# Kernel tuning notes

Measured on AMD Instinct MI355X. Metric: run time of the kernel, lower is better.

## Reference

```python
import jax, jax.numpy as jnp
import numpy as np
from functools import partial

BIG = 1e9  # placeholder squared distance for 'no surface voxel here'


def _surface(fg):
    """Boundary voxels: foreground with at least one 4-neighbor background (image border counts as background)."""
    p = jnp.pad(fg, 1)  # pads with False
    interior = p[:-2, 1:-1] & p[2:, 1:-1] & p[1:-1, :-2] & p[1:-1, 2:]
    return fg & ~interior


def _edt(mask):
    """Exact Euclidean distance transform (unit spacing, matching spacing_mm=(1,1,1)).
    Separable two-pass: 1D squared distance along rows, then combine along columns.
    mask: [H, W] bool -> dist: [H, W] float32 distance to nearest True voxel."""
    H, W = mask.shape
    i = jnp.arange(H, dtype=jnp.float32)
    j = jnp.arange(W, dtype=jnp.float32)
    d1 = (i[:, None] - i[None, :]) ** 2                      # [H, H]
    pen = jnp.where(mask, 0.0, BIG).astype(jnp.float32)      # [H, W]
    g = jnp.min(d1[:, :, None] + pen[None, :, :], axis=1)    # [H, W] (min over source row i')
    d2 = (j[:, None] - j[None, :]) ** 2                      # [W, W]
    f = jnp.min(g[:, None, :] + d2[None, :, :], axis=2)      # [H, W] (min over source col j')
    return jnp.sqrt(f)


def _percentile(d, mask, pct):
    """pct-percentile of d over voxels where mask is True (inf if mask empty)."""
    vals = jnp.sort(jnp.where(mask, d, jnp.inf).ravel())
    n = jnp.sum(mask)
    idx = jnp.clip(jnp.ceil(pct / 100.0 * n.astype(jnp.float32)).astype(jnp.int32) - 1,
                   0, vals.size - 1)
    return jnp.where(n > 0, vals[idx], jnp.inf)


def _pair_hd(pred_m, gt_m):
    """Robust Hausdorff (100th and 95th percentile) between surfaces of two binary masks."""
    sp = _surface(pred_m)
    sg = _surface(gt_m)
    dt_to_pred = _edt(sp)  # distance of every voxel to pred surface
    dt_to_gt = _edt(sg)    # distance of every voxel to gt surface

    def robust(p):
        return jnp.maximum(_percentile(dt_to_pred, sg, p),   # gt -> pred
                           _percentile(dt_to_gt, sp, p))     # pred -> gt

    return jnp.stack([robust(100.0), robust(95.0)])  # [2]


def _forward(logits, target):
    num_classes = logits.shape[1]
    probs = jax.nn.softmax(logits, axis=1)
    pred = jnp.argmax(probs, axis=1)  # [B, H, W]
    classes = jnp.arange(1, num_classes)  # include_background=False -> drop class 0
    pred_oh = pred[:, None, :, :] == classes[None, :, None, None]    # [B, Cfg, H, W] bool
    tgt_oh = target[:, None, :, :] == classes[None, :, None, None]   # [B, Cfg, H, W] bool

    def per_image(args):
        pm, tm = args  # each [Cfg, H, W]
        return jax.vmap(_pair_hd)(pm, tm)  # [Cfg, 2]

    res = jax.lax.map(per_image, (pred_oh, tgt_oh))  # [B, Cfg, 2]
    # average='micro': mean over all (batch, class) pairs
    return jnp.mean(res, axis=(0, 1))  # [2] = (hd100, hd95)


def setup_inputs() -> dict:
    key = jax.random.key(0)
    k1, k2 = jax.random.split(key)
    B, C, H, W = 8, 4, 192, 192
    logits = jax.random.normal(k1, (B, C, H, W), dtype=jnp.float32)
    target = jax.random.randint(k2, (B, H, W), 0, C, dtype=jnp.int64)
    return {"logits": logits, "target": target}


def reference(logits, target):
    return _forward(logits, target)
```

## Files before the change

### kernel.cpp

```cpp
#include <hip/hip_runtime.h>
#include <hip/hip_bf16.h>
#include <math.h>
#include <stdint.h>
#include <limits.h>

#define BB 8
#define NC 4
#define HH 192
#define WW 192
#define HWP (HH * WW)
#define NPAIR 24
#define NPD 48
#define NWRD 576
#define NCHUNK 16
#define WPC (NWRD / NCHUNK)
#define NBIN 4096
#define BIGI 1000000000

typedef unsigned long long u64;

__global__ void k_prep(const float* __restrict__ logits, const int* __restrict__ target,
                       u64* __restrict__ fgbits, unsigned* __restrict__ ghist,
                       int* __restrict__ ovfcnt, int* __restrict__ ovfmax) {
    int idx = blockIdx.x * 256 + threadIdx.x;
    if (idx < NPD * NBIN) ghist[idx] = 0;
    if (blockIdx.x == 1151) {
        if (threadIdx.x < NPD) ovfcnt[threadIdx.x] = 0;
        else if (threadIdx.x >= 64 && threadIdx.x < 64 + NPD) ovfmax[threadIdx.x - 64] = 0;
    }
    int b = idx / HWP;
    int p = idx - b * HWP;
    const float* base = logits + (size_t)b * NC * HWP + p;
    float l0 = base[0], l1 = base[HWP], l2 = base[2 * HWP], l3 = base[3 * HWP];
    int pred = 0; float best = l0;
    if (l1 > best) { best = l1; pred = 1; }
    if (l2 > best) { best = l2; pred = 2; }
    if (l3 > best) { best = l3; pred = 3; }
    int t = target[(size_t)b * HWP + p];
    int lane = threadIdx.x & 63;
    int g = p >> 6;
#pragma unroll
    for (int cls = 1; cls <= 3; ++cls) {
        u64 mp = __ballot(pred == cls);
        u64 mt = __ballot(t == cls);
        if (lane == 0) {
            int pair = b * 3 + (cls - 1);
            fgbits[(size_t)(pair * 2 + 0) * NWRD + g] = mp;
            fgbits[(size_t)(pair * 2 + 1) * NWRD + g] = mt;
        }
    }
}

__device__ __forceinline__ u64 surf_word(const u64* F, int i, int k) {
    u64 r0 = F[i * 3], r1 = F[i * 3 + 1], r2 = F[i * 3 + 2];
    u64 r = F[i * 3 + k];
    u64 u = (i > 0) ? F[(i - 1) * 3 + k] : 0ull;
    u64 d = (i < HH - 1) ? F[(i + 1) * 3 + k] : 0ull;
    u64 lf, rt;
    if (k == 0)      { lf = r0 << 1;                rt = (r0 >> 1) | (r1 << 63); }
    else if (k == 1) { lf = (r1 << 1) | (r0 >> 63); rt = (r1 >> 1) | (r2 << 63); }
    else             { lf = (r2 << 1) | (r1 >> 63); rt = r2 >> 1; }
    return r & ~(u & d & lf & rt);
}

__device__ __forceinline__ int rowdist(const u64* w, int j) {
    int qw = j >> 6, qb2 = j & 63;
    int dr = INT_MAX, dl = INT_MAX;
    u64 m = w[qw] & (~0ull << qb2);
    if (m) dr = ((qw << 6) + __ffsll(m) - 1) - j;
    else {
        for (int k = qw + 1; k < 3; ++k)
            if (w[k]) { dr = ((k << 6) + __ffsll(w[k]) - 1) - j; break; }
    }
    u64 ml = w[qw] & (~0ull >> (63 - qb2));
    if (ml) dl = j - ((qw << 6) + 63 - __clzll((long long)ml));
    else {
        for (int k = qw - 1; k >= 0; --k)
            if (w[k]) { dl = j - ((k << 6) + 63 - __clzll((long long)w[k])); break; }
    }
    return min(dl, dr);
}

__global__ __launch_bounds__(256) void k_query(const u64* __restrict__ fgbits,
                        unsigned* __restrict__ ghist, int* __restrict__ ovfval,
                        int* __restrict__ ovfcnt, int* __restrict__ ovfmax) {
    int chunk = blockIdx.x, pd = blockIdx.y, qpd = pd ^ 1;
    int tid = threadIdx.x;
    __shared__ u64 sF[NWRD];
    __shared__ u64 sG[NWRD];
    __shared__ u64 sS[NWRD];
    __shared__ uint16_t qb[WPC * 64];
    __shared__ unsigned shist[NBIN];
    __shared__ int wcnt[WPC + 1];

    for (int t = tid; t < NWRD; t += 256) {
        sF[t] = fgbits[(size_t)pd * NWRD + t];
        sG[t] = fgbits[(size_t)qpd * NWRD + t];
    }
    for (int t = tid; t < NBIN; t += 256) shist[t] = 0;
    __syncthreads();
    for (int w = tid; w < NWRD; w += 256) sS[w] = surf_word(sF, w / 3, w % 3);

    u64 myq = 0;
    if (tid < WPC) {
        int w = chunk * WPC + tid;
        myq = surf_word(sG, w / 3, w % 3);
        wcnt[tid] = __popcll(myq);
    }
    __syncthreads();
    if (tid == 0) {
        int acc = 0;
        for (int w = 0; w < WPC; ++w) { int c = wcnt[w]; wcnt[w] = acc; acc += c; }
        wcnt[WPC] = acc;
    }
    __syncthreads();
    if (tid < WPC) {
        int w = chunk * WPC + tid;
        int i = w / 3, k = w % 3;
        int off = wcnt[tid];
        u64 m = myq;
        while (m) { int bi = __ffsll(m) - 1; m &= m - 1; qb[off++] = (uint16_t)((i << 8) | (k * 64 + bi)); }
    }
    __syncthreads();

    int nq = wcnt[WPC];
    for (int q = tid; q < nq; q += 256) {
        int e = qb[q];
        int qi = e >> 8, qj = e & 255;
        int best = BIGI;
        for (int s = 0; s < HH; ++s) {
            if (s * s >= best) break;
            int r = qi - s;
            if (r >= 0) {
                int dj = rowdist(sS + r * 3, qj);
                if (dj != INT_MAX) best = min(best, s * s + dj * dj);
            }
            r = qi + s;
            if (s > 0 && r < HH) {
                int dj = rowdist(sS + r * 3, qj);
                if (dj != INT_MAX) best = min(best, s * s + dj * dj);
            }
        }
        if (best < NBIN) {
            atomicAdd(&shist[best], 1u);
        } else {
            int ix = atomicAdd(&ovfcnt[pd], 1);
            ovfval[(size_t)pd * HWP + ix] = best;
            atomicMax(&ovfmax[pd], best);
        }
    }
    __syncthreads();
    for (int bin = tid; bin < NBIN; bin += 256)
        if (shist[bin]) atomicAdd(&ghist[pd * NBIN + bin], shist[bin]);
}

__global__ __launch_bounds__(256) void k_sel(const unsigned* __restrict__ ghist,
                        const int* __restrict__ ovfval, const int* __restrict__ ovfcnt,
                        const int* __restrict__ ovfmax, float* __restrict__ res) {
    int pd = blockIdx.x, tid = threadIdx.x, lane = tid & 63, wid = tid >> 6;
    __shared__ int swt[4];
    __shared__ int sred[4];
    __shared__ int sv95;
    const unsigned* H = ghist + pd * NBIN;

    unsigned c[16];
    int s_t = 0;
#pragma unroll
    for (int u = 0; u < 16; ++u) { c[u] = H[tid * 16 + u]; s_t += (int)c[u]; }

    int inc = s_t;
    for (int off = 1; off < 64; off <<= 1) { int t = __shfl_up(inc, off); if (lane >= off) inc += t; }
    if (lane == 63) swt[wid] = inc;
    __syncthreads();
    int woff = 0;
    for (int w = 0; w < wid; ++w) woff += swt[w];
    int total = swt[0] + swt[1] + swt[2] + swt[3];
    int base = woff + inc - s_t;

    int novf = ovfcnt[pd];
    int n = total + novf;

    int mybin = -1;
#pragma unroll
    for (int u = 0; u < 16; ++u) if (c[u]) mybin = tid * 16 + u;
    for (int off = 32; off; off >>= 1) mybin = max(mybin, __shfl_down(mybin, off));
    if (lane == 0) sred[wid] = mybin;
    __syncthreads();
    int vmax = max(max(sred[0], sred[1]), max(sred[2], sred[3]));
    if (novf > 0) vmax = max(vmax, ovfmax[pd]);

    if (n == 0) {
        if (tid == 0) { res[pd * 2 + 0] = INFINITY; res[pd * 2 + 1] = INFINITY; }
        return;
    }
    int kk;
    { float kf = ceilf(0.95f * (float)n); kk = (int)kf; if (kk < 1) kk = 1; if (kk > n) kk = n; }

    if (kk <= total) {
        if (base < kk && kk <= base + s_t) {
            int cum = base;
#pragma unroll
            for (int u = 0; u < 16; ++u) {
                cum += (int)c[u];
                if (cum >= kk) { sv95 = tid * 16 + u; break; }
            }
        }
        __syncthreads();
        if (tid == 0) {
            res[pd * 2 + 0] = sqrtf((float)vmax);
            res[pd * 2 + 1] = sqrtf((float)sv95);
        }
    } else {
        int r = kk - total;
        const int* OV = ovfval + (size_t)pd * HWP;
        int lo = NBIN, hi = vmax;
        while (lo < hi) {
            int mid = lo + ((hi - lo) >> 1);
            int cc = 0;
            for (int k = tid; k < novf; k += 256) if (OV[k] <= mid) cc++;
            for (int off = 32; off; off >>= 1) cc += __shfl_down(cc, off);
            if (lane == 0) sred[wid] = cc;
            __syncthreads();
            int tot = sred[0] + sred[1] + sred[2] + sred[3];
            __syncthreads();
            if (tot >= r) hi = mid; else lo = mid + 1;
        }
        if (tid == 0) {
            res[pd * 2 + 0] = sqrtf((float)vmax);
            res[pd * 2 + 1] = sqrtf((float)lo);
        }
    }
}

__global__ void k_final(const float* __restrict__ res, float* __restrict__ out) {
    int tid = threadIdx.x;
    float v100 = 0.0f, v95 = 0.0f;
    if (tid < NPAIR) {
        v100 = fmaxf(res[tid * 4 + 0], res[tid * 4 + 2]);
        v95  = fmaxf(res[tid * 4 + 1], res[tid * 4 + 3]);
    }
    for (int off = 32; off; off >>= 1) {
        v100 += __shfl_down(v100, off);
        v95  += __shfl_down(v95, off);
    }
    if (tid == 0) {
        out[0] = v100 / (float)NPAIR;
        out[1] = v95 / (float)NPAIR;
    }
}

extern "C" void kernel_launch(void* const* d_in, const int* in_sizes, int n_in,
                              void* d_out, int out_size, void* d_ws, size_t ws_size,
                              hipStream_t stream) {
    const float* logits = (const float*)d_in[0];
    const int* target = (const int*)d_in[1];
    float* out = (float*)d_out;

    uint8_t* ws = (uint8_t*)d_ws;
    u64*      fgbits = (u64*)ws;
    unsigned* ghist  = (unsigned*)(ws + 221184);
    int*      ovfval = (int*)(ws + 1007616);
    int*      ovfcnt = (int*)(ws + 8085504);
    int*      ovfmax = (int*)(ws + 8085696);
    float*    res    = (float*)(ws + 8085888);

    k_prep<<<(BB * HWP) / 256, 256, 0, stream>>>(logits, target, fgbits, ghist, ovfcnt, ovfmax);
    k_query<<<dim3(NCHUNK, NPD), 256, 0, stream>>>(fgbits, ghist, ovfval, ovfcnt, ovfmax);
    k_sel<<<NPD, 256, 0, stream>>>(ghist, ovfval, ovfcnt, ovfmax, res);
    k_final<<<1, 64, 0, stream>>>(res, out);
}
```

Measured before the change: 75.50 us.

## Fuse selection and final averaging kernels, halve query chunk count

Merges the per-direction percentile selection and the final mean into one kernel, with one block per pair handling both directions and adding its contribution to the output atomically. The output is zeroed in the prep kernel, which removes one launch and the intermediate result buffer. The query grid is halved (NCHUNK 16→8), so each block handles more words and fewer shared histograms are flushed to global memory, at the cost of less parallelism. Float atomic accumulation makes the summation order nondeterministic.

After: 78.35 us. +3.8%, slower.

```diff
diff --git a/kernel.cpp b/kernel.cpp
--- a/kernel.cpp
+++ b/kernel.cpp
@@ -12,7 +12,7 @@
 #define NPAIR 24
 #define NPD 48
 #define NWRD 576
-#define NCHUNK 16
+#define NCHUNK 8
 #define WPC (NWRD / NCHUNK)
 #define NBIN 4096
 #define BIGI 1000000000
@@ -21,12 +21,14 @@
 
 __global__ void k_prep(const float* __restrict__ logits, const int* __restrict__ target,
                        u64* __restrict__ fgbits, unsigned* __restrict__ ghist,
-                       int* __restrict__ ovfcnt, int* __restrict__ ovfmax) {
+                       int* __restrict__ ovfcnt, int* __restrict__ ovfmax,
+                       float* __restrict__ out) {
     int idx = blockIdx.x * 256 + threadIdx.x;
     if (idx < NPD * NBIN) ghist[idx] = 0;
     if (blockIdx.x == 1151) {
         if (threadIdx.x < NPD) ovfcnt[threadIdx.x] = 0;
         else if (threadIdx.x >= 64 && threadIdx.x < 64 + NPD) ovfmax[threadIdx.x - 64] = 0;
+        else if (threadIdx.x >= 128 && threadIdx.x < 130) out[threadIdx.x - 128] = 0.0f;
     }
     int b = idx / HWP;
     int p = idx - b * HWP;
@@ -154,98 +156,91 @@
         if (shist[bin]) atomicAdd(&ghist[pd * NBIN + bin], shist[bin]);
 }
 
-__global__ __launch_bounds__(256) void k_sel(const unsigned* __restrict__ ghist,
+__global__ __launch_bounds__(256) void k_selfinal(const unsigned* __restrict__ ghist,
                         const int* __restrict__ ovfval, const int* __restrict__ ovfcnt,
-                        const int* __restrict__ ovfmax, float* __restrict__ res) {
-    int pd = blockIdx.x, tid = threadIdx.x, lane = tid & 63, wid = tid >> 6;
+                        const int* __restrict__ ovfmax, float* __restrict__ out) {
+    int pair = blockIdx.x, tid = threadIdx.x, lane = tid & 63, wid = tid >> 6;
     __shared__ int swt[4];
     __shared__ int sred[4];
     __shared__ int sv95;
-    const unsigned* H = ghist + pd * NBIN;
-
-    unsigned c[16];
-    int s_t = 0;
-#pragma unroll
-    for (int u = 0; u < 16; ++u) { c[u] = H[tid * 16 + u]; s_t += (int)c[u]; }
-
-    int inc = s_t;
-    for (int off = 1; off < 64; off <<= 1) { int t = __shfl_up(inc, off); if (lane >= off) inc += t; }
-    if (lane == 63) swt[wid] = inc;
-    __syncthreads();
-    int woff = 0;
-    for (int w = 0; w < wid; ++w) woff += swt[w];
-    int total = swt[0] + swt[1] + swt[2] + swt[3];
-    int base = woff + inc - s_t;
-
-    int novf = ovfcnt[pd];
-    int n = total + novf;
-
-    int mybin = -1;
-#pragma unroll
-    for (int u = 0; u < 16; ++u) if (c[u]) mybin = tid * 16 + u;
-    for (int off = 32; off; off >>= 1) mybin = max(mybin, __shfl_down(mybin, off));
-    if (lane == 0) sred[wid] = mybin;
-    __syncthreads();
-    int vmax = max(max(sred[0], sred[1]), max(sred[2], sred[3]));
-    if (novf > 0) vmax = max(vmax, ovfmax[pd]);
-
-    if (n == 0) {
-        if (tid == 0) { res[pd * 2 + 0] = INFINITY; res[pd * 2 + 1] = INFINITY; }
-        return;
-    }
-    int kk;
-    { float kf = ceilf(0.95f * (float)n); kk = (int)kf; if (kk < 1) kk = 1; if (kk > n) kk = n; }
-
-    if (kk <= total) {
-        if (base < kk && kk <= base + s_t) {
-            int cum = base;
-#pragma unroll
-            for (int u = 0; u < 16; ++u) {
-                cum += (int)c[u];
-                if (cum >= kk) { sv95 = tid * 16 + u; break; }
+    __shared__ float sr[4];
+
+    for (int d = 0; d < 2; ++d) {
+        int pd = pair * 2 + d;
+        const unsigned* H = ghist + pd * NBIN;
+
+        unsigned c[16];
+        int s_t = 0;
+#pragma unroll
+        for (int u = 0; u < 16; ++u) { c[u] = H[tid * 16 + u]; s_t += (int)c[u]; }
+
+        int inc = s_t;
+        for (int off = 1; off < 64; off <<= 1) { int t = __shfl_up(inc, off); if (lane >= off) inc += t; }
+        if (lane == 63) swt[wid] = inc;
+        __syncthreads();
+        int woff = 0;
+        for (int w = 0; w < wid; ++w) woff += swt[w];
+        int total = swt[0] + swt[1] + swt[2] + swt[3];
+        int base = woff + inc - s_t;
+
+        int novf = ovfcnt[pd];
+        int n = total + novf;
+
+        int mybin = -1;
+#pragma unroll
+        for (int u = 0; u < 16; ++u) if (c[u]) mybin = tid * 16 + u;
+        for (int off = 32; off; off >>= 1) mybin = max(mybin, __shfl_down(mybin, off));
+        if (lane == 0) sred[wid] = mybin;
+        __syncthreads();
+        int vmax = max(max(sred[0], sred[1]), max(sred[2], sred[3]));
+        if (novf > 0) vmax = max(vmax, ovfmax[pd]);
+        __syncthreads();
+
+        float r100, r95;
+        if (n == 0) {
+            r100 = INFINITY; r95 = INFINITY;
+        } else {
+            int kk;
+            { float kf = ceilf(0.95f * (float)n); kk = (int)kf; if (kk < 1) kk = 1; if (kk > n) kk = n; }
+            r100 = sqrtf((float)vmax);
+            if (kk <= total) {
+                if (base < kk && kk <= base + s_t) {
+                    int cum = base;
+#pragma unroll
+                    for (int u = 0; u < 16; ++u) {
+                        cum += (int)c[u];
+                        if (cum >= kk) { sv95 = tid * 16 + u; break; }
+                    }
+                }
+                __syncthreads();
+                r95 = sqrtf((float)sv95);
+            } else {
+                int r = kk - total;
+                const int* OV = ovfval + (size_t)pd * HWP;
+                int lo = NBIN, hi = vmax;
+                while (lo < hi) {
+                    int mid = lo + ((hi - lo) >> 1);
+                    int cc = 0;
+                    for (int k = tid; k < novf; k += 256) if (OV[k] <= mid) cc++;
+                    for (int off = 32; off; off >>= 1) cc += __shfl_down(cc, off);
+                    if (lane == 0) sred[wid] = cc;
+                    __syncthreads();
+                    int tot = sred[0] + sred[1] + sred[2] + sred[3];
+                    __syncthreads();
+                    if (tot >= r) hi = mid; else lo = mid + 1;
+                }
+                r95 = sqrtf((float)lo);
             }
         }
-        __syncthreads();
-        if (tid == 0) {
-            res[pd * 2 + 0] = sqrtf((float)vmax);
-            res[pd * 2 + 1] = sqrtf((float)sv95);
-        }
-    } else {
-        int r = kk - total;
-        const int* OV = ovfval + (size_t)pd * HWP;
-        int lo = NBIN, hi = vmax;
-        while (lo < hi) {
-            int mid = lo + ((hi - lo) >> 1);
-            int cc = 0;
-            for (int k = tid; k < novf; k += 256) if (OV[k] <= mid) cc++;
-            for (int off = 32; off; off >>= 1) cc += __shfl_down(cc, off);
-            if (lane == 0) sred[wid] = cc;
-            __syncthreads();
-            int tot = sred[0] + sred[1] + sred[2] + sred[3];
-            __syncthreads();
-            if (tot >= r) hi = mid; else lo = mid + 1;
-        }
-        if (tid == 0) {
-            res[pd * 2 + 0] = sqrtf((float)vmax);
-            res[pd * 2 + 1] = sqrtf((float)lo);
-        }
-    }
-}
-
-__global__ void k_final(const float* __restrict__ res, float* __restrict__ out) {
-    int tid = threadIdx.x;
-    float v100 = 0.0f, v95 = 0.0f;
-    if (tid < NPAIR) {
-        v100 = fmaxf(res[tid * 4 + 0], res[tid * 4 + 2]);
-        v95  = fmaxf(res[tid * 4 + 1], res[tid * 4 + 3]);
-    }
-    for (int off = 32; off; off >>= 1) {
-        v100 += __shfl_down(v100, off);
-        v95  += __shfl_down(v95, off);
-    }
+        if (tid == 0) { sr[d] = r100; sr[2 + d] = r95; }
+        __syncthreads();
+    }
+
     if (tid == 0) {
-        out[0] = v100 / (float)NPAIR;
-        out[1] = v95 / (float)NPAIR;
+        float v100 = fmaxf(sr[0], sr[1]);
+        float v95  = fmaxf(sr[2], sr[3]);
+        atomicAdd(&out[0], v100 * (1.0f / NPAIR));
+        atomicAdd(&out[1], v95  * (1.0f / NPAIR));
     }
 }
 
@@ -264,8 +259,8 @@
     int*      ovfmax = (int*)(ws + 8085696);
     float*    res    = (float*)(ws + 8085888);
 
-    k_prep<<<(BB * HWP) / 256, 256, 0, stream>>>(logits, target, fgbits, ghist, ovfcnt, ovfmax);
+    (void)res;
+    k_prep<<<(BB * HWP) / 256, 256, 0, stream>>>(logits, target, fgbits, ghist, ovfcnt, ovfmax, out);
     k_query<<<dim3(NCHUNK, NPD), 256, 0, stream>>>(fgbits, ghist, ovfval, ovfcnt, ovfmax);
-    k_sel<<<NPD, 256, 0, stream>>>(ghist, ovfval, ovfcnt, ovfmax, res);
-    k_final<<<1, 64, 0, stream>>>(res, out);
-}
+    k_selfinal<<<NPAIR, 256, 0, stream>>>(ghist, ovfval, ovfcnt, ovfmax, out);
+}
```
